# Performance work log

Measured on AMD Instinct MI355X. Metric: run time of the kernel, lower is better.

The kernel has to match this reference:

```python
import jax, jax.numpy as jnp
import numpy as np

N_NODES = 100000
N_EDGES = 800000
D = 32           # output_dim == node feature dim
D_EDGE = 32      # embedded edge feature dim
H = 64           # psi hidden units
PSI_IN = 4 * D + D_EDGE  # 160


def setup_inputs() -> dict:
    key = jax.random.key(0)
    ks = jax.random.split(key, 12)
    inp = {
        "h_d_prev": jax.random.normal(ks[0], (N_NODES, D), dtype=jnp.float32),
        "h_s": jax.random.normal(ks[1], (N_NODES, D), dtype=jnp.float32),
        "edge_features_embedded": jax.random.normal(ks[2], (N_EDGES, D_EDGE), dtype=jnp.float32),
        "sender_indices": jax.random.randint(ks[3], (N_EDGES,), 0, N_NODES, dtype=jnp.int32),
        "receiver_indices": jax.random.randint(ks[4], (N_EDGES,), 0, N_NODES, dtype=jnp.int32),
        # psi MLP params (Dense with relu on every layer, incl. last since final_activation=None)
        "psi_w0": jax.random.normal(ks[5], (PSI_IN, H), dtype=jnp.float32) * (1.0 / np.sqrt(PSI_IN)),
        "psi_b0": jnp.zeros((H,), dtype=jnp.float32),
        "psi_w1": jax.random.normal(ks[6], (H, H), dtype=jnp.float32) * (1.0 / np.sqrt(H)),
        "psi_b1": jnp.zeros((H,), dtype=jnp.float32),
        "psi_w2": jax.random.normal(ks[7], (H, D), dtype=jnp.float32) * (1.0 / np.sqrt(H)),
        "psi_b2": jnp.zeros((D,), dtype=jnp.float32),
        # final W matrix (Dense, no bias)
        "W": jax.random.normal(ks[8], (D, D), dtype=jnp.float32) * (1.0 / np.sqrt(D)),
    }
    return inp


def reference(h_d_prev, h_s, edge_features_embedded, sender_indices, receiver_indices,
              psi_w0, psi_b0, psi_w1, psi_b1, psi_w2, psi_b2, W):
    # Gather node features onto edges
    h_di = h_d_prev[sender_indices]      # [E, D]
    h_dj = h_d_prev[receiver_indices]    # [E, D]
    h_si = h_s[sender_indices]           # [E, D]
    h_sj = h_s[receiver_indices]         # [E, D]

    psi_in = jnp.concatenate([h_si, h_sj, h_di, h_dj, edge_features_embedded], axis=-1)  # [E, 4D+De]
    x = jax.nn.relu(psi_in @ psi_w0 + psi_b0)
    x = jax.nn.relu(x @ psi_w1 + psi_b1)
    psi_out = jax.nn.relu(x @ psi_w2 + psi_b2)  # [E, D]

    s_ij = psi_out * (h_dj - h_di)  # [E, D]
    aggregated = jax.ops.segment_sum(s_ij, receiver_indices, num_segments=h_d_prev.shape[0])  # [N, D]
    return h_d_prev + aggregated @ W
```

## Files before the change

### kernel.cpp

```cpp
#include <hip/hip_runtime.h>

#define DD 32
#define HH 64

typedef __attribute__((ext_vector_type(8))) short bf16x8;
typedef __attribute__((ext_vector_type(4))) float f32x4;

static __device__ __forceinline__ unsigned short f2bf(float x) {
    union { float f; unsigned u; } v; v.f = x;
    unsigned r = (v.u + 0x7FFFu + ((v.u >> 16) & 1u)) >> 16;
    return (unsigned short)r;
}

__global__ __launch_bounds__(256) void prep_weights(
    const float* __restrict__ w0, const float* __restrict__ w1,
    const float* __restrict__ w2, unsigned short* __restrict__ frags)
{
    const int tid = blockIdx.x * 256 + threadIdx.x;
    const int f = tid >> 6, l = tid & 63;
    if (f >= 32) return;
    const int c = l & 15, q = l >> 4;
    unsigned short* dst = frags + f * 512 + l * 8;
    if (f < 20) {
        const int kk = f >> 2, t = f & 3;
        const int n = t * 16 + c, kb = kk * 32 + q * 8;
        #pragma unroll
        for (int j = 0; j < 8; ++j) dst[j] = f2bf(w0[(kb + j) * HH + n]);
    } else if (f < 28) {
        const int f2 = f - 20, kk = f2 >> 2, t = f2 & 3;
        const int n = t * 16 + c, kb = kk * 32 + q * 8;
        #pragma unroll
        for (int j = 0; j < 8; ++j) dst[j] = f2bf(w1[(kb + j) * HH + n]);
    } else {
        const int f3 = f - 28, kk = f3 >> 1, t = f3 & 1;
        const int n = t * 16 + c, kb = kk * 32 + q * 8;
        #pragma unroll
        for (int j = 0; j < 8; ++j) dst[j] = f2bf(w2[(kb + j) * DD + n]);
    }
}

__global__ __launch_bounds__(256, 2) void edge_mfma(
    const float* __restrict__ h_d, const float* __restrict__ h_s,
    const float* __restrict__ ef,
    const int* __restrict__ snd, const int* __restrict__ rcv,
    const unsigned short* __restrict__ frags,
    const float* __restrict__ b0, const float* __restrict__ b1,
    const float* __restrict__ b2,
    float* __restrict__ agg, int E, int ntiles)
{
    __shared__ __align__(16) unsigned short xbuf[4][2][16 * 72];

    const int lane = threadIdx.x & 63;
    const int w = threadIdx.x >> 6;
    const int c = lane & 15, q = lane >> 4;

    bf16x8 wf[32];
    #pragma unroll
    for (int f = 0; f < 32; ++f)
        wf[f] = *(const bf16x8*)(frags + f * 512 + lane * 8);

    const float b0t[4] = {b0[c], b0[16 + c], b0[32 + c], b0[48 + c]};
    const float b1t[4] = {b1[c], b1[16 + c], b1[32 + c], b1[48 + c]};
    const float b2t[2] = {b2[c], b2[16 + c]};

    unsigned short* xb1 = xbuf[w][0];
    unsigned short* xb2 = xbuf[w][1];

    const int wave_id = blockIdx.x * 4 + w;
    const int nwaves = gridDim.x * 4;

    for (int tile = wave_id; tile < ntiles; tile += nwaves) {
        const int base = tile * 16;
        int e = base + c; if (e >= E) e = E - 1;
        const int si = snd[e], ri = rcv[e];
        const float* srcs[5] = { h_s + (size_t)si * DD, h_s + (size_t)ri * DD,
                                 h_d + (size_t)si * DD, h_d + (size_t)ri * DD,
                                 ef  + (size_t)e  * DD };

        f32x4 c0[4] = {f32x4{0,0,0,0}, f32x4{0,0,0,0}, f32x4{0,0,0,0}, f32x4{0,0,0,0}};
        #pragma unroll
        for (int kk = 0; kk < 5; ++kk) {
            const float* s = srcs[kk] + q * 8;
            const float4 v0 = ((const float4*)s)[0];
            const float4 v1 = ((const float4*)s)[1];
            bf16x8 a;
            a[0] = (short)f2bf(v0.x); a[1] = (short)f2bf(v0.y);
            a[2] = (short)f2bf(v0.z); a[3] = (short)f2bf(v0.w);
            a[4] = (short)f2bf(v1.x); a[5] = (short)f2bf(v1.y);
            a[6] = (short)f2bf(v1.z); a[7] = (short)f2bf(v1.w);
            #pragma unroll
            for (int t = 0; t < 4; ++t)
                c0[t] = __builtin_amdgcn_mfma_f32_16x16x32_bf16(a, wf[kk * 4 + t], c0[t], 0, 0, 0);
        }
        #pragma unroll
        for (int t = 0; t < 4; ++t) {
            #pragma unroll
            for (int r = 0; r < 4; ++r) {
                const float v = fmaxf(c0[t][r] + b0t[t], 0.0f);
                xb1[(q * 4 + r) * 72 + t * 16 + c] = f2bf(v);
            }
        }

        f32x4 c1[4] = {f32x4{0,0,0,0}, f32x4{0,0,0,0}, f32x4{0,0,0,0}, f32x4{0,0,0,0}};
        #pragma unroll
        for (int kk = 0; kk < 2; ++kk) {
            const bf16x8 a = *(const bf16x8*)(xb1 + c * 72 + kk * 32 + q * 8);
            #pragma unroll
            for (int t = 0; t < 4; ++t)
                c1[t] = __builtin_amdgcn_mfma_f32_16x16x32_bf16(a, wf[20 + kk * 4 + t], c1[t], 0, 0, 0);
        }
        #pragma unroll
        for (int t = 0; t < 4; ++t) {
            #pragma unroll
            for (int r = 0; r < 4; ++r) {
                const float v = fmaxf(c1[t][r] + b1t[t], 0.0f);
                xb2[(q * 4 + r) * 72 + t * 16 + c] = f2bf(v);
            }
        }

        f32x4 c2[2] = {f32x4{0,0,0,0}, f32x4{0,0,0,0}};
        #pragma unroll
        for (int kk = 0; kk < 2; ++kk) {
            const bf16x8 a = *(const bf16x8*)(xb2 + c * 72 + kk * 32 + q * 8);
            #pragma unroll
            for (int t = 0; t < 2; ++t)
                c2[t] = __builtin_amdgcn_mfma_f32_16x16x32_bf16(a, wf[28 + kk * 2 + t], c2[t], 0, 0, 0);
        }

        int erv[4], sir[4], rir[4];
        #pragma unroll
        for (int r = 0; r < 4; ++r) {
            const int ee = base + q * 4 + r;
            erv[r] = ee;
            const int eec = ee < E ? ee : E - 1;
            sir[r] = snd[eec]; rir[r] = rcv[eec];
        }
        #pragma unroll
        for (int t = 0; t < 2; ++t) {
            const int h = t * 16 + c;
            #pragma unroll
            for (int r = 0; r < 4; ++r) {
                if (erv[r] < E) {
                    const float psi = fmaxf(c2[t][r] + b2t[t], 0.0f);
                    const float d = h_d[(size_t)rir[r] * DD + h] - h_d[(size_t)sir[r] * DD + h];
                    atomicAdd(agg + (size_t)rir[r] * DD + h, psi * d);
                }
            }
        }
    }
}

__global__ __launch_bounds__(256) void out_kernel(
    const float* __restrict__ h_d, const float* __restrict__ agg,
    const float* __restrict__ W, float* __restrict__ out, int N)
{
    const int idx = blockIdx.x * 256 + threadIdx.x;
    if (idx >= N * DD) return;
    const int n = idx >> 5;
    const int d = idx & 31;
    const float* arow = agg + (size_t)n * DD;
    float s = h_d[idx];
    #pragma unroll
    for (int k = 0; k < DD; ++k) s = fmaf(arow[k], W[k * DD + d], s);
    out[idx] = s;
}

extern "C" void kernel_launch(void* const* d_in, const int* in_sizes, int n_in,
                              void* d_out, int out_size, void* d_ws, size_t ws_size,
                              hipStream_t stream) {
    const float* h_d = (const float*)d_in[0];
    const float* h_s = (const float*)d_in[1];
    const float* ef  = (const float*)d_in[2];
    const int*   snd = (const int*)d_in[3];
    const int*   rcv = (const int*)d_in[4];
    const float* w0  = (const float*)d_in[5];
    const float* b0  = (const float*)d_in[6];
    const float* w1  = (const float*)d_in[7];
    const float* b1  = (const float*)d_in[8];
    const float* w2  = (const float*)d_in[9];
    const float* b2  = (const float*)d_in[10];
    const float* W   = (const float*)d_in[11];
    float* out = (float*)d_out;

    const int N = in_sizes[0] / DD;
    const int E = in_sizes[3];
    const int ntiles = (E + 15) / 16;

    float* agg = (float*)d_ws;
    unsigned short* frags = (unsigned short*)((char*)d_ws + (size_t)N * DD * sizeof(float));

    hipMemsetAsync(agg, 0, (size_t)N * DD * sizeof(float), stream);
    prep_weights<<<8, 256, 0, stream>>>(w0, w1, w2, frags);
    edge_mfma<<<1024, 256, 0, stream>>>(h_d, h_s, ef, snd, rcv, frags,
                                        b0, b1, b2, agg, E, ntiles);
    out_kernel<<<((N * DD) + 255) / 256, 256, 0, stream>>>(h_d, agg, W, out, N);
}
```

Measured before the change: 367.7 us.

## Transpose MFMA operands to chain MLP layers in registers, drop LDS staging

```diff
diff --git a/kernel.cpp b/kernel.cpp
--- a/kernel.cpp
+++ b/kernel.cpp
@@ -1,4 +1,5 @@
 #include <hip/hip_runtime.h>
+#include <hip/hip_bf16.h>
 
 #define DD 32
 #define HH 64
@@ -8,8 +9,12 @@
 
 static __device__ __forceinline__ unsigned short f2bf(float x) {
     union { float f; unsigned u; } v; v.f = x;
-    unsigned r = (v.u + 0x7FFFu + ((v.u >> 16) & 1u)) >> 16;
-    return (unsigned short)r;
+    return (unsigned short)((v.u + 0x7FFFu + ((v.u >> 16) & 1u)) >> 16);
+}
+
+static __device__ __forceinline__ unsigned pk2(float a, float b) {
+    __hip_bfloat162 h = __float22bfloat162_rn(make_float2(a, b));
+    union { __hip_bfloat162 h2; unsigned u; } cv; cv.h2 = h; return cv.u;
 }
 
 __global__ __launch_bounds__(256) void prep_weights(
@@ -22,20 +27,29 @@
     const int c = l & 15, q = l >> 4;
     unsigned short* dst = frags + f * 512 + l * 8;
     if (f < 20) {
-        const int kk = f >> 2, t = f & 3;
-        const int n = t * 16 + c, kb = kk * 32 + q * 8;
-        #pragma unroll
-        for (int j = 0; j < 8; ++j) dst[j] = f2bf(w0[(kb + j) * HH + n]);
+        const int t = f / 5, kk = f % 5;
+        const int m = t * 16 + c;
+        #pragma unroll
+        for (int j = 0; j < 8; ++j) {
+            const int k = kk * 32 + q * 8 + j;
+            dst[j] = f2bf(w0[k * HH + m]);
+        }
     } else if (f < 28) {
-        const int f2 = f - 20, kk = f2 >> 2, t = f2 & 3;
-        const int n = t * 16 + c, kb = kk * 32 + q * 8;
-        #pragma unroll
-        for (int j = 0; j < 8; ++j) dst[j] = f2bf(w1[(kb + j) * HH + n]);
+        const int f1 = f - 20, t = f1 >> 1, kp = f1 & 1;
+        const int m = t * 16 + c;
+        #pragma unroll
+        for (int j = 0; j < 8; ++j) {
+            const int k = kp * 32 + (j >> 2) * 16 + q * 4 + (j & 3);
+            dst[j] = f2bf(w1[k * HH + m]);
+        }
     } else {
-        const int f3 = f - 28, kk = f3 >> 1, t = f3 & 1;
-        const int n = t * 16 + c, kb = kk * 32 + q * 8;
-        #pragma unroll
-        for (int j = 0; j < 8; ++j) dst[j] = f2bf(w2[(kb + j) * DD + n]);
+        const int f2i = f - 28, t = f2i >> 1, kp = f2i & 1;
+        const int m = t * 16 + c;
+        #pragma unroll
+        for (int j = 0; j < 8; ++j) {
+            const int k = kp * 32 + (j >> 2) * 16 + q * 4 + (j & 3);
+            dst[j] = f2bf(w2[k * DD + m]);
+        }
     }
 }
 
@@ -48,102 +62,108 @@
     const float* __restrict__ b2,
     float* __restrict__ agg, int E, int ntiles)
 {
-    __shared__ __align__(16) unsigned short xbuf[4][2][16 * 72];
-
     const int lane = threadIdx.x & 63;
-    const int w = threadIdx.x >> 6;
     const int c = lane & 15, q = lane >> 4;
 
-    bf16x8 wf[32];
-    #pragma unroll
-    for (int f = 0; f < 32; ++f)
-        wf[f] = *(const bf16x8*)(frags + f * 512 + lane * 8);
-
-    const float b0t[4] = {b0[c], b0[16 + c], b0[32 + c], b0[48 + c]};
-    const float b1t[4] = {b1[c], b1[16 + c], b1[32 + c], b1[48 + c]};
-    const float b2t[2] = {b2[c], b2[16 + c]};
-
-    unsigned short* xb1 = xbuf[w][0];
-    unsigned short* xb2 = xbuf[w][1];
-
-    const int wave_id = blockIdx.x * 4 + w;
+    bf16x8 wf0[20];
+    #pragma unroll
+    for (int f = 0; f < 20; ++f) wf0[f] = *(const bf16x8*)(frags + f * 512 + lane * 8);
+    bf16x8 wf1[8];
+    #pragma unroll
+    for (int f = 0; f < 8; ++f) wf1[f] = *(const bf16x8*)(frags + 10240 + f * 512 + lane * 8);
+    bf16x8 wf2[4];
+    #pragma unroll
+    for (int f = 0; f < 4; ++f) wf2[f] = *(const bf16x8*)(frags + 14336 + f * 512 + lane * 8);
+
+    f32x4 b0v[4], b1v[4], b2v[2];
+    #pragma unroll
+    for (int t = 0; t < 4; ++t) b0v[t] = *(const f32x4*)(b0 + t * 16 + q * 4);
+    #pragma unroll
+    for (int t = 0; t < 4; ++t) b1v[t] = *(const f32x4*)(b1 + t * 16 + q * 4);
+    #pragma unroll
+    for (int t = 0; t < 2; ++t) b2v[t] = *(const f32x4*)(b2 + t * 16 + q * 4);
+
+    const int wave_id = blockIdx.x * 4 + (threadIdx.x >> 6);
     const int nwaves = gridDim.x * 4;
 
     for (int tile = wave_id; tile < ntiles; tile += nwaves) {
         const int base = tile * 16;
-        int e = base + c; if (e >= E) e = E - 1;
+        int e = base + c;
+        const bool valid = (e < E);
+        if (!valid) e = E - 1;
         const int si = snd[e], ri = rcv[e];
-        const float* srcs[5] = { h_s + (size_t)si * DD, h_s + (size_t)ri * DD,
-                                 h_d + (size_t)si * DD, h_d + (size_t)ri * DD,
-                                 ef  + (size_t)e  * DD };
-
-        f32x4 c0[4] = {f32x4{0,0,0,0}, f32x4{0,0,0,0}, f32x4{0,0,0,0}, f32x4{0,0,0,0}};
+
+        const float* s0 = h_s + (size_t)si * DD;
+        const float* s1 = h_s + (size_t)ri * DD;
+        const float* s2 = h_d + (size_t)si * DD;
+        const float* s3 = h_d + (size_t)ri * DD;
+        const float* s4 = ef  + (size_t)e  * DD;
+
+        f32x4 di[2], dj[2];
+        #pragma unroll
+        for (int t = 0; t < 2; ++t) {
+            di[t] = *(const f32x4*)(s2 + t * 16 + q * 4);
+            dj[t] = *(const f32x4*)(s3 + t * 16 + q * 4);
+        }
+
+        f32x4 c0[4] = {b0v[0], b0v[1], b0v[2], b0v[3]};
+        const float* srcs[5] = {s0, s1, s2, s3, s4};
         #pragma unroll
         for (int kk = 0; kk < 5; ++kk) {
-            const float* s = srcs[kk] + q * 8;
-            const float4 v0 = ((const float4*)s)[0];
-            const float4 v1 = ((const float4*)s)[1];
-            bf16x8 a;
-            a[0] = (short)f2bf(v0.x); a[1] = (short)f2bf(v0.y);
-            a[2] = (short)f2bf(v0.z); a[3] = (short)f2bf(v0.w);
-            a[4] = (short)f2bf(v1.x); a[5] = (short)f2bf(v1.y);
-            a[6] = (short)f2bf(v1.z); a[7] = (short)f2bf(v1.w);
+            const f32x4 u0 = *(const f32x4*)(srcs[kk] + q * 8);
+            const f32x4 u1 = *(const f32x4*)(srcs[kk] + q * 8 + 4);
+            union { unsigned u[4]; bf16x8 v; } bb;
+            bb.u[0] = pk2(u0[0], u0[1]); bb.u[1] = pk2(u0[2], u0[3]);
+            bb.u[2] = pk2(u1[0], u1[1]); bb.u[3] = pk2(u1[2], u1[3]);
             #pragma unroll
             for (int t = 0; t < 4; ++t)
-                c0[t] = __builtin_amdgcn_mfma_f32_16x16x32_bf16(a, wf[kk * 4 + t], c0[t], 0, 0, 0);
-        }
-        #pragma unroll
-        for (int t = 0; t < 4; ++t) {
-            #pragma unroll
-            for (int r = 0; r < 4; ++r) {
-                const float v = fmaxf(c0[t][r] + b0t[t], 0.0f);
-                xb1[(q * 4 + r) * 72 + t * 16 + c] = f2bf(v);
-            }
-        }
-
-        f32x4 c1[4] = {f32x4{0,0,0,0}, f32x4{0,0,0,0}, f32x4{0,0,0,0}, f32x4{0,0,0,0}};
-        #pragma unroll
-        for (int kk = 0; kk < 2; ++kk) {
-            const bf16x8 a = *(const bf16x8*)(xb1 + c * 72 + kk * 32 + q * 8);
+                c0[t] = __builtin_amdgcn_mfma_f32_16x16x32_bf16(wf0[t * 5 + kk], bb.v, c0[t], 0, 0, 0);
+        }
+
+        unsigned x1[4][2];
+        #pragma unroll
+        for (int kt = 0; kt < 4; ++kt) {
+            x1[kt][0] = pk2(fmaxf(c0[kt][0], 0.f), fmaxf(c0[kt][1], 0.f));
+            x1[kt][1] = pk2(fmaxf(c0[kt][2], 0.f), fmaxf(c0[kt][3], 0.f));
+        }
+
+        f32x4 c1[4] = {b1v[0], b1v[1], b1v[2], b1v[3]};
+        #pragma unroll
+        for (int kp = 0; kp < 2; ++kp) {
+            union { unsigned u[4]; bf16x8 v; } bb;
+            bb.u[0] = x1[2 * kp][0];     bb.u[1] = x1[2 * kp][1];
+            bb.u[2] = x1[2 * kp + 1][0]; bb.u[3] = x1[2 * kp + 1][1];
             #pragma unroll
             for (int t = 0; t < 4; ++t)
-                c1[t] = __builtin_amdgcn_mfma_f32_16x16x32_bf16(a, wf[20 + kk * 4 + t], c1[t], 0, 0, 0);
-        }
-        #pragma unroll
-        for (int t = 0; t < 4; ++t) {
-            #pragma unroll
-            for (int r = 0; r < 4; ++r) {
-                const float v = fmaxf(c1[t][r] + b1t[t], 0.0f);
-                xb2[(q * 4 + r) * 72 + t * 16 + c] = f2bf(v);
-            }
-        }
-
-        f32x4 c2[2] = {f32x4{0,0,0,0}, f32x4{0,0,0,0}};
-        #pragma unroll
-        for (int kk = 0; kk < 2; ++kk) {
-            const bf16x8 a = *(const bf16x8*)(xb2 + c * 72 + kk * 32 + q * 8);
+                c1[t] = __builtin_amdgcn_mfma_f32_16x16x32_bf16(wf1[t * 2 + kp], bb.v, c1[t], 0, 0, 0);
+        }
+
+        unsigned x2[4][2];
+        #pragma unroll
+        for (int kt = 0; kt < 4; ++kt) {
+            x2[kt][0] = pk2(fmaxf(c1[kt][0], 0.f), fmaxf(c1[kt][1], 0.f));
+            x2[kt][1] = pk2(fmaxf(c1[kt][2], 0.f), fmaxf(c1[kt][3], 0.f));
+        }
+
+        f32x4 c2[2] = {b2v[0], b2v[1]};
+        #pragma unroll
+        for (int kp = 0; kp < 2; ++kp) {
+            union { unsigned u[4]; bf16x8 v; } bb;
+            bb.u[0] = x2[2 * kp][0];     bb.u[1] = x2[2 * kp][1];
+            bb.u[2] = x2[2 * kp + 1][0]; bb.u[3] = x2[2 * kp + 1][1];
             #pragma unroll
             for (int t = 0; t < 2; ++t)
-                c2[t] = __builtin_amdgcn_mfma_f32_16x16x32_bf16(a, wf[28 + kk * 2 + t], c2[t], 0, 0, 0);
-        }
-
-        int erv[4], sir[4], rir[4];
-        #pragma unroll
-        for (int r = 0; r < 4; ++r) {
-            const int ee = base + q * 4 + r;
-            erv[r] = ee;
-            const int eec = ee < E ? ee : E - 1;
-            sir[r] = snd[eec]; rir[r] = rcv[eec];
-        }
-        #pragma unroll
-        for (int t = 0; t < 2; ++t) {
-            const int h = t * 16 + c;
-            #pragma unroll
-            for (int r = 0; r < 4; ++r) {
-                if (erv[r] < E) {
-                    const float psi = fmaxf(c2[t][r] + b2t[t], 0.0f);
-                    const float d = h_d[(size_t)rir[r] * DD + h] - h_d[(size_t)sir[r] * DD + h];
-                    atomicAdd(agg + (size_t)rir[r] * DD + h, psi * d);
+                c2[t] = __builtin_amdgcn_mfma_f32_16x16x32_bf16(wf2[t * 2 + kp], bb.v, c2[t], 0, 0, 0);
+        }
+
+        if (valid) {
+            float* ar = agg + (size_t)ri * DD + q * 4;
+            #pragma unroll
+            for (int t = 0; t < 2; ++t) {
+                #pragma unroll
+                for (int r = 0; r < 4; ++r) {
+                    const float psi = fmaxf(c2[t][r], 0.f);
+                    atomicAdd(ar + t * 16 + r, psi * (dj[t][r] - di[t][r]));
                 }
             }
         }
@@ -154,15 +174,26 @@
     const float* __restrict__ h_d, const float* __restrict__ agg,
     const float* __restrict__ W, float* __restrict__ out, int N)
 {
-    const int idx = blockIdx.x * 256 + threadIdx.x;
-    if (idx >= N * DD) return;
-    const int n = idx >> 5;
-    const int d = idx & 31;
-    const float* arow = agg + (size_t)n * DD;
-    float s = h_d[idx];
-    #pragma unroll
-    for (int k = 0; k < DD; ++k) s = fmaf(arow[k], W[k * DD + d], s);
-    out[idx] = s;
+    const int n = blockIdx.x * 256 + threadIdx.x;
+    if (n >= N) return;
+    const f32x4* ar = (const f32x4*)(agg + (size_t)n * DD);
+    const f32x4* hr = (const f32x4*)(h_d + (size_t)n * DD);
+    float a[DD], o[DD];
+    #pragma unroll
+    for (int i = 0; i < 8; ++i) {
+        const f32x4 av = ar[i], hv = hr[i];
+        a[4 * i] = av[0]; a[4 * i + 1] = av[1]; a[4 * i + 2] = av[2]; a[4 * i + 3] = av[3];
+        o[4 * i] = hv[0]; o[4 * i + 1] = hv[1]; o[4 * i + 2] = hv[2]; o[4 * i + 3] = hv[3];
+    }
+    #pragma unroll
+    for (int k = 0; k < DD; ++k) {
+        const float ak = a[k];
+        #pragma unroll
+        for (int d = 0; d < DD; ++d) o[d] = fmaf(ak, W[k * DD + d], o[d]);
+    }
+    f32x4* ov = (f32x4*)(out + (size_t)n * DD);
+    #pragma unroll
+    for (int i = 0; i < 8; ++i) ov[i] = f32x4{o[4 * i], o[4 * i + 1], o[4 * i + 2], o[4 * i + 3]};
 }
 
 extern "C" void kernel_launch(void* const* d_in, const int* in_sizes, int n_in,
@@ -193,5 +224,5 @@
     prep_weights<<<8, 256, 0, stream>>>(w0, w1, w2, frags);
     edge_mfma<<<1024, 256, 0, stream>>>(h_d, h_s, ef, snd, rcv, frags,
                                         b0, b1, b2, agg, E, ntiles);
-    out_kernel<<<((N * DD) + 255) / 256, 256, 0, stream>>>(h_d, agg, W, out, N);
-}
+    out_kernel<<<(N + 255) / 256, 256, 0, stream>>>(h_d, agg, W, out, N);
+}
```

Result: slower. 516.2 us (+40.4%).
